# Kernel tuning notes

Hardware: AMD Instinct MI355X
Metric: run time of the kernel (lower is better)

Reference implementation:

```python
import jax, jax.numpy as jnp
import numpy as np

N = 12288
C = 1            # n_channels_r
FEAT = 44        # features_dim
RES = 20         # RESIDUE_TYPES_N


def _lin_params(key, fan_in, fan_out):
    k1, k2 = jax.random.split(key)
    bound = 1.0 / np.sqrt(fan_in)
    W = jax.random.uniform(k1, (fan_in, fan_out), minval=-bound, maxval=bound, dtype=jnp.float32)
    b = jax.random.uniform(k2, (fan_out,), minval=-bound, maxval=bound, dtype=jnp.float32)
    return W, b


def setup_inputs() -> dict:
    key = jax.random.key(0)
    ks = jax.random.split(key, 20)
    inp = {
        'one_hot': jax.random.uniform(ks[0], (N, RES), dtype=jnp.float32),
        'features': jax.random.normal(ks[1], (N, FEAT), dtype=jnp.float32),
        'gemme_features': jax.random.normal(ks[2], (N, 1), dtype=jnp.float32),
        'a_res': jax.random.uniform(ks[3], (C, N, N), dtype=jnp.float32),
    }
    # encoder MLP
    inp['We1'], inp['be1'] = _lin_params(ks[4], RES + FEAT, 32)
    inp['We2'], inp['be2'] = _lin_params(ks[5], 32, 64)
    inp['We3'], inp['be3'] = _lin_params(ks[6], 64, 128)
    # graph conv weights: per-relation-channel [C, in, out]
    dims = [(128, 64), (64, 32), (32, 16), (16, 8), (8, 4)]
    for i, (di, do) in enumerate(dims):
        k1, k2 = jax.random.split(ks[7 + i])
        bound = 1.0 / np.sqrt(di)
        inp[f'Wg{i+1}'] = jax.random.uniform(k1, (C, di, do), minval=-bound, maxval=bound, dtype=jnp.float32)
        inp[f'bg{i+1}'] = jax.random.uniform(k2, (do,), minval=-bound, maxval=bound, dtype=jnp.float32)
    # final MLP
    inp['Wf1'], inp['bf1'] = _lin_params(ks[12], 4, 8)
    inp['Wf2'], inp['bf2'] = _lin_params(ks[13], 8, 4)
    inp['Wf3'], inp['bf3'] = _lin_params(ks[14], 4, 1)
    return inp


def _gconv(x, A, W, b):
    # x: [N, in], A: [C, N, N], W: [C, in, out]
    h = jnp.einsum('ni,cio->cno', x, W)          # per-channel linear
    y = jnp.einsum('cmn,cno->mo', A, h) + b      # neighbor aggregation, sum over channels
    return jax.nn.elu(y)


def reference(one_hot, features, gemme_features, a_res,
              We1, be1, We2, be2, We3, be3,
              Wg1, bg1, Wg2, bg2, Wg3, bg3, Wg4, bg4, Wg5, bg5,
              Wf1, bf1, Wf2, bf2, Wf3, bf3):
    x = jnp.concatenate([one_hot, features], axis=1)       # [N, 64]
    x = jax.nn.elu(x @ We1 + be1)                           # dropout = identity (eval)
    x = jax.nn.elu(x @ We2 + be2)
    x = jax.nn.elu(x @ We3 + be3)                           # [N, 128]
    x = _gconv(x, a_res, Wg1, bg1)
    x = _gconv(x, a_res, Wg2, bg2)
    x = _gconv(x, a_res, Wg3, bg3)
    x = _gconv(x, a_res, Wg4, bg4)
    x = _gconv(x, a_res, Wg5, bg5)                          # [N, 4]
    x = jax.nn.elu(x @ Wf1 + bf1)
    x = jax.nn.elu(x @ Wf2 + bf2)
    return jax.nn.sigmoid(x @ Wf3 + bf3)                    # [N, 1]
```

## Files before the change

### kernel.cpp

```cpp
#include <hip/hip_runtime.h>
#include <math.h>

#define NROWS 12288

__device__ __forceinline__ float elu_f(float x) { return x > 0.f ? x : expm1f(x); }

__global__ __launch_bounds__(256) void enc1_kernel(
    const float* __restrict__ oh, const float* __restrict__ ft,
    const float* __restrict__ W, const float* __restrict__ b,
    float* __restrict__ out)
{
    int id = blockIdx.x * 256 + threadIdx.x;
    if (id >= NROWS * 8) return;
    int o4 = id & 7;
    int m  = id >> 3;
    const float4* W4 = reinterpret_cast<const float4*>(W);
    float4 acc = reinterpret_cast<const float4*>(b)[o4];
    const float* ohr = oh + m * 20;
    const float* ftr = ft + m * 44;
#pragma unroll
    for (int i = 0; i < 64; ++i) {
        float x = (i < 20) ? ohr[i] : ftr[i - 20];
        float4 w = W4[i * 8 + o4];
        acc.x = fmaf(x, w.x, acc.x);
        acc.y = fmaf(x, w.y, acc.y);
        acc.z = fmaf(x, w.z, acc.z);
        acc.w = fmaf(x, w.w, acc.w);
    }
    acc.x = elu_f(acc.x); acc.y = elu_f(acc.y);
    acc.z = elu_f(acc.z); acc.w = elu_f(acc.w);
    reinterpret_cast<float4*>(out)[id] = acc;
}

template <int IN, int OUT, bool BIAS, bool ACT_ELU>
__global__ __launch_bounds__(256) void linear4_kernel(
    const float* __restrict__ in, const float* __restrict__ W,
    const float* __restrict__ b, float* __restrict__ out)
{
    constexpr int O4 = OUT / 4;
    int id = blockIdx.x * 256 + threadIdx.x;
    if (id >= NROWS * O4) return;
    int o4 = id % O4;
    int m  = id / O4;
    float4 acc;
    if (BIAS) acc = reinterpret_cast<const float4*>(b)[o4];
    else      acc = make_float4(0.f, 0.f, 0.f, 0.f);
    const float*  ip = in + (size_t)m * IN;
    const float4* W4 = reinterpret_cast<const float4*>(W);
#pragma unroll 8
    for (int i = 0; i < IN; ++i) {
        float  x = ip[i];
        float4 w = W4[i * O4 + o4];
        acc.x = fmaf(x, w.x, acc.x);
        acc.y = fmaf(x, w.y, acc.y);
        acc.z = fmaf(x, w.z, acc.z);
        acc.w = fmaf(x, w.w, acc.w);
    }
    if (ACT_ELU) {
        acc.x = elu_f(acc.x); acc.y = elu_f(acc.y);
        acc.z = elu_f(acc.z); acc.w = elu_f(acc.w);
    }
    reinterpret_cast<float4*>(out)[id] = acc;
}

template <int OUT, int TM, int TN>
__global__ __launch_bounds__(256, 3) void agg_kernel(
    const float* __restrict__ A, const float* __restrict__ h,
    float* __restrict__ part)
{
    constexpr int BK = 32, BM = 256, SPLIT = 16;
    constexpr int TCOLS = OUT / TN;
    constexpr int TROWS = 256 / TCOLS;
    static_assert(TROWS * TM == BM, "tile mismatch");
    constexpr int MT  = NROWS / BM;
    constexpr int SEG = NROWS / SPLIT;
    constexpr int NT  = SEG / BK;
    constexpr int HV  = BK * OUT / 4;
    constexpr int HL  = (HV + 255) / 256;

    __shared__ float At[BK][BM];
    __shared__ float Hs[BK][OUT];

    const int tid = threadIdx.x;
    const int mt  = blockIdx.x % MT;
    const int seg = blockIdx.x / MT;
    const int m0  = mt * BM;
    const int kb  = seg * SEG;

    const int r0 = tid >> 3;
    const int c4 = tid & 7;
    const int tcol = tid % TCOLS;
    const int trow = tid / TCOLS;

    const float* Abase = A + (size_t)(m0 + r0) * NROWS + c4 * 4;

    float4 av[8];
    float4 hv[HL];

    auto load_tile = [&](int k0) {
#pragma unroll
        for (int p = 0; p < 8; ++p)
            av[p] = *reinterpret_cast<const float4*>(Abase + (size_t)(p * 32) * NROWS + k0);
        const float4* hsrc = reinterpret_cast<const float4*>(h + (size_t)k0 * OUT);
#pragma unroll
        for (int i = 0; i < HL; ++i)
            if (HV >= 256 * (i + 1) || i * 256 + tid < HV) hv[i] = hsrc[i * 256 + tid];
    };

    float acc[TM][TN];
#pragma unroll
    for (int i = 0; i < TM; ++i)
#pragma unroll
        for (int j = 0; j < TN; ++j) acc[i][j] = 0.f;

    load_tile(kb);

    for (int t = 0; t < NT; ++t) {
        __syncthreads();
        const int sw = c4 * 4;
#pragma unroll
        for (int p = 0; p < 8; ++p) {
            const int md = (r0 + p * 32) ^ sw;
            At[sw + 0][md] = av[p].x;
            At[sw + 1][md] = av[p].y;
            At[sw + 2][md] = av[p].z;
            At[sw + 3][md] = av[p].w;
        }
        float4* hdst = reinterpret_cast<float4*>(&Hs[0][0]);
#pragma unroll
        for (int i = 0; i < HL; ++i)
            if (HV >= 256 * (i + 1) || i * 256 + tid < HV) hdst[i * 256 + tid] = hv[i];
        __syncthreads();

        if (t + 1 < NT) load_tile(kb + (t + 1) * BK);

#pragma unroll
        for (int kk = 0; kk < BK; ++kk) {
            const int s24 = kk & 24, s4 = kk & 4;
            float af[TM];
            if constexpr (TM == 8) {
                const int base8 = (trow * 8) ^ s24;
                float4 a0 = *reinterpret_cast<const float4*>(&At[kk][base8 + s4]);
                float4 a1 = *reinterpret_cast<const float4*>(&At[kk][base8 + (s4 ^ 4)]);
                af[0] = a0.x; af[1] = a0.y; af[2] = a0.z; af[3] = a0.w;
                af[4] = a1.x; af[5] = a1.y; af[6] = a1.z; af[7] = a1.w;
            } else {
                const int b4 = (trow * 4) ^ (s24 | s4);
                float4 a0 = *reinterpret_cast<const float4*>(&At[kk][b4]);
                af[0] = a0.x; af[1] = a0.y; af[2] = a0.z; af[3] = a0.w;
            }
            float hf[TN];
            if constexpr (TN == 8) {
                float4 b0 = *reinterpret_cast<const float4*>(&Hs[kk][tcol * 8]);
                float4 b1 = *reinterpret_cast<const float4*>(&Hs[kk][tcol * 8 + 4]);
                hf[0] = b0.x; hf[1] = b0.y; hf[2] = b0.z; hf[3] = b0.w;
                hf[4] = b1.x; hf[5] = b1.y; hf[6] = b1.z; hf[7] = b1.w;
            } else if constexpr (TN == 4) {
                float4 b0 = *reinterpret_cast<const float4*>(&Hs[kk][tcol * 4]);
                hf[0] = b0.x; hf[1] = b0.y; hf[2] = b0.z; hf[3] = b0.w;
            } else if constexpr (TN == 2) {
                float2 b0 = *reinterpret_cast<const float2*>(&Hs[kk][tcol * 2]);
                hf[0] = b0.x; hf[1] = b0.y;
            } else {
                hf[0] = Hs[kk][tcol];
            }
#pragma unroll
            for (int i = 0; i < TM; ++i)
#pragma unroll
                for (int j = 0; j < TN; ++j)
                    acc[i][j] = fmaf(af[i], hf[j], acc[i][j]);
        }
    }

    float* pd = part + (size_t)seg * ((size_t)NROWS * OUT);
#pragma unroll
    for (int i = 0; i < TM; ++i) {
        const int m = m0 + trow * TM + i;
        float* row = pd + (size_t)m * OUT + tcol * TN;
        if constexpr (TN == 8) {
            *reinterpret_cast<float4*>(row)     = make_float4(acc[i][0], acc[i][1], acc[i][2], acc[i][3]);
            *reinterpret_cast<float4*>(row + 4) = make_float4(acc[i][4], acc[i][5], acc[i][6], acc[i][7]);
        } else if constexpr (TN == 4) {
            *reinterpret_cast<float4*>(row) = make_float4(acc[i][0], acc[i][1], acc[i][2], acc[i][3]);
        } else if constexpr (TN == 2) {
            *reinterpret_cast<float2*>(row) = make_float2(acc[i][0], acc[i][1]);
        } else {
            row[0] = acc[i][0];
        }
    }
}

template <int OUT, int SPLIT>
__global__ __launch_bounds__(256) void reduce_kernel(
    const float* __restrict__ part, const float* __restrict__ b,
    float* __restrict__ out)
{
    constexpr int O4 = OUT / 4;
    int id = blockIdx.x * 256 + threadIdx.x;
    if (id >= NROWS * O4) return;
    const float4* p4 = reinterpret_cast<const float4*>(part);
    float4 s = p4[id];
#pragma unroll
    for (int t = 1; t < SPLIT; ++t) {
        float4 v = p4[(size_t)t * (NROWS * O4) + id];
        s.x += v.x; s.y += v.y; s.z += v.z; s.w += v.w;
    }
    float4 bb = reinterpret_cast<const float4*>(b)[id % O4];
    s.x = elu_f(s.x + bb.x); s.y = elu_f(s.y + bb.y);
    s.z = elu_f(s.z + bb.z); s.w = elu_f(s.w + bb.w);
    reinterpret_cast<float4*>(out)[id] = s;
}

__global__ __launch_bounds__(256) void reduce5_final_kernel(
    const float* __restrict__ part, const float* __restrict__ bg,
    const float* __restrict__ Wf1, const float* __restrict__ bf1,
    const float* __restrict__ Wf2, const float* __restrict__ bf2,
    const float* __restrict__ Wf3, const float* __restrict__ bf3,
    float* __restrict__ out)
{
    int m = blockIdx.x * 256 + threadIdx.x;
    if (m >= NROWS) return;
    const float4* p4 = reinterpret_cast<const float4*>(part);
    float4 s = p4[m];
#pragma unroll
    for (int t = 1; t < 16; ++t) {
        float4 v = p4[(size_t)t * NROWS + m];
        s.x += v.x; s.y += v.y; s.z += v.z; s.w += v.w;
    }
    float x0 = elu_f(s.x + bg[0]);
    float x1 = elu_f(s.y + bg[1]);
    float x2 = elu_f(s.z + bg[2]);
    float x3 = elu_f(s.w + bg[3]);

    float t1[8];
#pragma unroll
    for (int o = 0; o < 8; ++o) {
        float a = bf1[o];
        a = fmaf(x0, Wf1[0 * 8 + o], a);
        a = fmaf(x1, Wf1[1 * 8 + o], a);
        a = fmaf(x2, Wf1[2 * 8 + o], a);
        a = fmaf(x3, Wf1[3 * 8 + o], a);
        t1[o] = elu_f(a);
    }
    float t2[4];
#pragma unroll
    for (int o = 0; o < 4; ++o) {
        float a = bf2[o];
#pragma unroll
        for (int i = 0; i < 8; ++i) a = fmaf(t1[i], Wf2[i * 4 + o], a);
        t2[o] = elu_f(a);
    }
    float z = bf3[0];
#pragma unroll
    for (int i = 0; i < 4; ++i) z = fmaf(t2[i], Wf3[i], z);
    out[m] = 1.f / (1.f + expf(-z));
}

static inline dim3 grid_for(int threads) { return dim3((threads + 255) / 256); }

extern "C" void kernel_launch(void* const* d_in, const int* in_sizes, int n_in,
                              void* d_out, int out_size, void* d_ws, size_t ws_size,
                              hipStream_t stream)
{
    (void)in_sizes; (void)n_in; (void)out_size; (void)ws_size;

    const float* one_hot  = (const float*)d_in[0];
    const float* features = (const float*)d_in[1];
    const float* A    = (const float*)d_in[3];
    const float* We1  = (const float*)d_in[4];  const float* be1 = (const float*)d_in[5];
    const float* We2  = (const float*)d_in[6];  const float* be2 = (const float*)d_in[7];
    const float* We3  = (const float*)d_in[8];  const float* be3 = (const float*)d_in[9];
    const float* Wg1  = (const float*)d_in[10]; const float* bg1 = (const float*)d_in[11];
    const float* Wg2  = (const float*)d_in[12]; const float* bg2 = (const float*)d_in[13];
    const float* Wg3  = (const float*)d_in[14]; const float* bg3 = (const float*)d_in[15];
    const float* Wg4  = (const float*)d_in[16]; const float* bg4 = (const float*)d_in[17];
    const float* Wg5  = (const float*)d_in[18]; const float* bg5 = (const float*)d_in[19];
    const float* Wf1  = (const float*)d_in[20]; const float* bf1 = (const float*)d_in[21];
    const float* Wf2  = (const float*)d_in[22]; const float* bf2 = (const float*)d_in[23];
    const float* Wf3  = (const float*)d_in[24]; const float* bf3 = (const float*)d_in[25];
    float* out = (float*)d_out;

    float* bufA = (float*)d_ws;
    float* bufB = bufA + (size_t)NROWS * 128;
    float* hb   = bufB + (size_t)NROWS * 128;
    float* part = hb   + (size_t)NROWS * 64;

    const dim3 agrid(48 * 16);

    enc1_kernel<<<grid_for(NROWS * 8), 256, 0, stream>>>(one_hot, features, We1, be1, bufB);
    linear4_kernel<32, 64, true, true><<<grid_for(NROWS * 16), 256, 0, stream>>>(bufB, We2, be2, bufA);
    linear4_kernel<64, 128, true, true><<<grid_for(NROWS * 32), 256, 0, stream>>>(bufA, We3, be3, bufB);

    linear4_kernel<128, 64, false, false><<<grid_for(NROWS * 16), 256, 0, stream>>>(bufB, Wg1, nullptr, hb);
    agg_kernel<64, 8, 8><<<agrid, 256, 0, stream>>>(A, hb, part);
    reduce_kernel<64, 16><<<grid_for(NROWS * 16), 256, 0, stream>>>(part, bg1, bufA);

    linear4_kernel<64, 32, false, false><<<grid_for(NROWS * 8), 256, 0, stream>>>(bufA, Wg2, nullptr, hb);
    agg_kernel<32, 8, 4><<<agrid, 256, 0, stream>>>(A, hb, part);
    reduce_kernel<32, 16><<<grid_for(NROWS * 8), 256, 0, stream>>>(part, bg2, bufB);

    linear4_kernel<32, 16, false, false><<<grid_for(NROWS * 4), 256, 0, stream>>>(bufB, Wg3, nullptr, hb);
    agg_kernel<16, 8, 2><<<agrid, 256, 0, stream>>>(A, hb, part);
    reduce_kernel<16, 16><<<grid_for(NROWS * 4), 256, 0, stream>>>(part, bg3, bufA);

    linear4_kernel<16, 8, false, false><<<grid_for(NROWS * 2), 256, 0, stream>>>(bufA, Wg4, nullptr, hb);
    agg_kernel<8, 8, 1><<<agrid, 256, 0, stream>>>(A, hb, part);
    reduce_kernel<8, 16><<<grid_for(NROWS * 2), 256, 0, stream>>>(part, bg4, bufB);

    linear4_kernel<8, 4, false, false><<<grid_for(NROWS), 256, 0, stream>>>(bufB, Wg5, nullptr, hb);
    agg_kernel<4, 4, 1><<<agrid, 256, 0, stream>>>(A, hb, part);
    reduce5_final_kernel<<<grid_for(NROWS), 256, 0, stream>>>(part, bg5, Wf1, bf1, Wf2, bf2, Wf3, bf3, out);
}
```

Baseline: 2.022 ms.

## Halve aggregation K-tile and retile threads to be wide across output columns

The A-tile depth in the adjacency aggregation kernel drops from 32 to 16, so each row is loaded by 4 threads with float4 reads instead of 8, and a new XOR swizzle is applied to the transposed shared-memory tile. The narrow layers switch from many rows per thread with few output columns to few rows with 8 (or 4) output columns, and TM=1/2/4 read paths are added. The goal is to cut registers and shared memory per block and to change the balance of shared-memory reads to FMAs. The cost is shorter contiguous global segments per row (64B instead of 128B) and twice as many barrier-separated iterations on a kernel that streams the large A matrix.

Result: no change. 2.039 ms (+0.8%).

```diff
diff --git a/kernel.cpp b/kernel.cpp
--- a/kernel.cpp
+++ b/kernel.cpp
@@ -68,7 +68,7 @@
     const float* __restrict__ A, const float* __restrict__ h,
     float* __restrict__ part)
 {
-    constexpr int BK = 32, BM = 256, SPLIT = 16;
+    constexpr int BK = 16, BM = 256, SPLIT = 16;
     constexpr int TCOLS = OUT / TN;
     constexpr int TROWS = 256 / TCOLS;
     static_assert(TROWS * TM == BM, "tile mismatch");
@@ -76,7 +76,6 @@
     constexpr int SEG = NROWS / SPLIT;
     constexpr int NT  = SEG / BK;
     constexpr int HV  = BK * OUT / 4;
-    constexpr int HL  = (HV + 255) / 256;
 
     __shared__ float At[BK][BM];
     __shared__ float Hs[BK][OUT];
@@ -87,24 +86,22 @@
     const int m0  = mt * BM;
     const int kb  = seg * SEG;
 
-    const int r0 = tid >> 3;
-    const int c4 = tid & 7;
+    const int r0 = tid >> 2;
+    const int c4 = tid & 3;
     const int tcol = tid % TCOLS;
     const int trow = tid / TCOLS;
 
     const float* Abase = A + (size_t)(m0 + r0) * NROWS + c4 * 4;
 
-    float4 av[8];
-    float4 hv[HL];
+    float4 av[4];
+    float4 hv;
 
     auto load_tile = [&](int k0) {
 #pragma unroll
-        for (int p = 0; p < 8; ++p)
-            av[p] = *reinterpret_cast<const float4*>(Abase + (size_t)(p * 32) * NROWS + k0);
-        const float4* hsrc = reinterpret_cast<const float4*>(h + (size_t)k0 * OUT);
-#pragma unroll
-        for (int i = 0; i < HL; ++i)
-            if (HV >= 256 * (i + 1) || i * 256 + tid < HV) hv[i] = hsrc[i * 256 + tid];
+        for (int p = 0; p < 4; ++p)
+            av[p] = *reinterpret_cast<const float4*>(Abase + (size_t)(p * 64) * NROWS + k0);
+        if (HV >= 256 || tid < HV)
+            hv = reinterpret_cast<const float4*>(h + (size_t)k0 * OUT)[tid];
     };
 
     float acc[TM][TN];
@@ -117,37 +114,38 @@
 
     for (int t = 0; t < NT; ++t) {
         __syncthreads();
-        const int sw = c4 * 4;
-#pragma unroll
-        for (int p = 0; p < 8; ++p) {
-            const int md = (r0 + p * 32) ^ sw;
-            At[sw + 0][md] = av[p].x;
-            At[sw + 1][md] = av[p].y;
-            At[sw + 2][md] = av[p].z;
-            At[sw + 3][md] = av[p].w;
+        const int kk0 = c4 * 4;
+#pragma unroll
+        for (int p = 0; p < 4; ++p) {
+            const int r = r0 + p * 64;
+            At[kk0 + 0][r ^ (((kk0 + 0) & 7) * 4)] = av[p].x;
+            At[kk0 + 1][r ^ (((kk0 + 1) & 7) * 4)] = av[p].y;
+            At[kk0 + 2][r ^ (((kk0 + 2) & 7) * 4)] = av[p].z;
+            At[kk0 + 3][r ^ (((kk0 + 3) & 7) * 4)] = av[p].w;
         }
-        float4* hdst = reinterpret_cast<float4*>(&Hs[0][0]);
-#pragma unroll
-        for (int i = 0; i < HL; ++i)
-            if (HV >= 256 * (i + 1) || i * 256 + tid < HV) hdst[i * 256 + tid] = hv[i];
+        if (HV >= 256 || tid < HV)
+            reinterpret_cast<float4*>(&Hs[0][0])[tid] = hv;
         __syncthreads();
 
         if (t + 1 < NT) load_tile(kb + (t + 1) * BK);
 
 #pragma unroll
         for (int kk = 0; kk < BK; ++kk) {
-            const int s24 = kk & 24, s4 = kk & 4;
+            const int S = (kk & 7) * 4;
             float af[TM];
             if constexpr (TM == 8) {
-                const int base8 = (trow * 8) ^ s24;
-                float4 a0 = *reinterpret_cast<const float4*>(&At[kk][base8 + s4]);
-                float4 a1 = *reinterpret_cast<const float4*>(&At[kk][base8 + (s4 ^ 4)]);
+                float4 a0 = *reinterpret_cast<const float4*>(&At[kk][(trow * 8) ^ S]);
+                float4 a1 = *reinterpret_cast<const float4*>(&At[kk][((trow * 8) + 4) ^ S]);
                 af[0] = a0.x; af[1] = a0.y; af[2] = a0.z; af[3] = a0.w;
                 af[4] = a1.x; af[5] = a1.y; af[6] = a1.z; af[7] = a1.w;
+            } else if constexpr (TM == 4) {
+                float4 a0 = *reinterpret_cast<const float4*>(&At[kk][(trow * 4) ^ S]);
+                af[0] = a0.x; af[1] = a0.y; af[2] = a0.z; af[3] = a0.w;
+            } else if constexpr (TM == 2) {
+                float2 a0 = *reinterpret_cast<const float2*>(&At[kk][(trow * 2) ^ S]);
+                af[0] = a0.x; af[1] = a0.y;
             } else {
-                const int b4 = (trow * 4) ^ (s24 | s4);
-                float4 a0 = *reinterpret_cast<const float4*>(&At[kk][b4]);
-                af[0] = a0.x; af[1] = a0.y; af[2] = a0.z; af[3] = a0.w;
+                af[0] = At[kk][trow ^ S];
             }
             float hf[TN];
             if constexpr (TN == 8) {
@@ -155,14 +153,9 @@
                 float4 b1 = *reinterpret_cast<const float4*>(&Hs[kk][tcol * 8 + 4]);
                 hf[0] = b0.x; hf[1] = b0.y; hf[2] = b0.z; hf[3] = b0.w;
                 hf[4] = b1.x; hf[5] = b1.y; hf[6] = b1.z; hf[7] = b1.w;
-            } else if constexpr (TN == 4) {
+            } else {
                 float4 b0 = *reinterpret_cast<const float4*>(&Hs[kk][tcol * 4]);
                 hf[0] = b0.x; hf[1] = b0.y; hf[2] = b0.z; hf[3] = b0.w;
-            } else if constexpr (TN == 2) {
-                float2 b0 = *reinterpret_cast<const float2*>(&Hs[kk][tcol * 2]);
-                hf[0] = b0.x; hf[1] = b0.y;
-            } else {
-                hf[0] = Hs[kk][tcol];
             }
 #pragma unroll
             for (int i = 0; i < TM; ++i)
@@ -180,12 +173,8 @@
         if constexpr (TN == 8) {
             *reinterpret_cast<float4*>(row)     = make_float4(acc[i][0], acc[i][1], acc[i][2], acc[i][3]);
             *reinterpret_cast<float4*>(row + 4) = make_float4(acc[i][4], acc[i][5], acc[i][6], acc[i][7]);
-        } else if constexpr (TN == 4) {
+        } else {
             *reinterpret_cast<float4*>(row) = make_float4(acc[i][0], acc[i][1], acc[i][2], acc[i][3]);
-        } else if constexpr (TN == 2) {
-            *reinterpret_cast<float2*>(row) = make_float2(acc[i][0], acc[i][1]);
-        } else {
-            row[0] = acc[i][0];
         }
     }
 }
@@ -296,18 +285,18 @@
     reduce_kernel<64, 16><<<grid_for(NROWS * 16), 256, 0, stream>>>(part, bg1, bufA);
 
     linear4_kernel<64, 32, false, false><<<grid_for(NROWS * 8), 256, 0, stream>>>(bufA, Wg2, nullptr, hb);
-    agg_kernel<32, 8, 4><<<agrid, 256, 0, stream>>>(A, hb, part);
+    agg_kernel<32, 4, 8><<<agrid, 256, 0, stream>>>(A, hb, part);
     reduce_kernel<32, 16><<<grid_for(NROWS * 8), 256, 0, stream>>>(part, bg2, bufB);
 
     linear4_kernel<32, 16, false, false><<<grid_for(NROWS * 4), 256, 0, stream>>>(bufB, Wg3, nullptr, hb);
-    agg_kernel<16, 8, 2><<<agrid, 256, 0, stream>>>(A, hb, part);
+    agg_kernel<16, 2, 8><<<agrid, 256, 0, stream>>>(A, hb, part);
     reduce_kernel<16, 16><<<grid_for(NROWS * 4), 256, 0, stream>>>(part, bg3, bufA);
 
     linear4_kernel<16, 8, false, false><<<grid_for(NROWS * 2), 256, 0, stream>>>(bufA, Wg4, nullptr, hb);
-    agg_kernel<8, 8, 1><<<agrid, 256, 0, stream>>>(A, hb, part);
+    agg_kernel<8, 1, 8><<<agrid, 256, 0, stream>>>(A, hb, part);
     reduce_kernel<8, 16><<<grid_for(NROWS * 2), 256, 0, stream>>>(part, bg4, bufB);
 
     linear4_kernel<8, 4, false, false><<<grid_for(NROWS), 256, 0, stream>>>(bufB, Wg5, nullptr, hb);
-    agg_kernel<4, 4, 1><<<agrid, 256, 0, stream>>>(A, hb, part);
+    agg_kernel<4, 1, 4><<<agrid, 256, 0, stream>>>(A, hb, part);
     reduce5_final_kernel<<<grid_for(NROWS), 256, 0, stream>>>(part, bg5, Wf1, bf1, Wf2, bf2, Wf3, bf3, out);
 }
```
